# Kernel tuning notes

Hardware: AMD Instinct MI355X
Metric: run time of the kernel (lower is better)

## Reference

```python
import jax, jax.numpy as jnp
import numpy as np

NB_NODE = 100000
FT = 256
OUT_FT = 256
NB_REL = 4
BATCH = 8192
DEG = 16  # padded neighbors per (node, relation)


def setup_inputs() -> dict:
    key = jax.random.key(0)
    k1, k2, k3, k4 = jax.random.split(key, 4)
    features = jax.random.normal(k1, (NB_NODE, FT), dtype=jnp.float32)
    neighbor_idx = jax.random.randint(k2, (BATCH, NB_REL, DEG), 0, NB_NODE, dtype=jnp.int32)
    # per-relation GCN weight, scaled like xavier
    W = jax.random.normal(k3, (NB_REL, FT, OUT_FT), dtype=jnp.float32) * (1.0 / np.sqrt(FT))
    b = jnp.zeros((NB_REL, OUT_FT), dtype=jnp.float32)
    prelu_a = jnp.full((1,), 0.25, dtype=jnp.float32)  # nn.PReLU() default single param
    node_list = jax.random.randint(k4, (BATCH,), 0, NB_NODE, dtype=jnp.int32)
    return {"features": features, "neighbor_idx": neighbor_idx, "W": W, "b": b,
            "prelu_a": prelu_a, "node_list": node_list, "k": 0}


def _prelu(x, a):
    return jnp.where(x >= 0, x, a * x)


def reference(features, neighbor_idx, W, b, prelu_a, node_list, k):
    # Ragged per-relation neighbor gather + mean (vectorized form of the
    # python double loop): [B, R, D, F] -> mean over D -> [B, R, F]
    v_in = jnp.mean(features[neighbor_idx], axis=2)
    # Per-relation GCN linear + PReLU: [B, R, F] x [R, F, O] -> [B, R, O]
    h = jnp.einsum('brf,rfo->bro', v_in, W) + b[None, :, :]
    h = _prelu(h, prelu_a[0])
    # isAtt=False branch: mean over relations -> [B, O]
    return jnp.mean(h, axis=1)
```

## Files before the change

kernel.cpp:

```cpp
#include <hip/hip_runtime.h>

#define B_TOT 8192
#define FT    256
#define NREL  4
#define DEG   16
#define BM    16

typedef __attribute__((ext_vector_type(8))) short bf16x8;
typedef __attribute__((ext_vector_type(4))) float f32x4;

static __device__ __forceinline__ unsigned short f2bf(float x) {
    union { float f; unsigned int u; } c; c.f = x;
    unsigned int u = c.u;
    u += 0x7fffu + ((u >> 16) & 1u);
    return (unsigned short)(u >> 16);
}
static __device__ __forceinline__ float bf2f(unsigned short h) {
    union { unsigned int u; float f; } c; c.u = ((unsigned int)h) << 16;
    return c.f;
}

__global__ __launch_bounds__(256) void cvt_feat_k(const float* __restrict__ f,
                                                  unsigned short* __restrict__ fb,
                                                  int n4) {
    int i = blockIdx.x * 256 + threadIdx.x;
    if (i < n4) {
        float4 x = ((const float4*)f)[i];
        ushort4 o;
        o.x = f2bf(x.x); o.y = f2bf(x.y); o.z = f2bf(x.z); o.w = f2bf(x.w);
        ((ushort4*)fb)[i] = o;
    }
}

__global__ __launch_bounds__(256) void wtrans_k(const float* __restrict__ W,
                                                unsigned short* __restrict__ Wt) {
    __shared__ float t[64][65];
    int r = blockIdx.z, ft = blockIdx.y, ot = blockIdx.x;
    int c = threadIdx.x & 63, rw = threadIdx.x >> 6;
    const float* src = W + ((size_t)r * 256 + ft * 64) * 256 + ot * 64;
#pragma unroll
    for (int i = 0; i < 16; ++i) {
        int row = i * 4 + rw;
        t[row][c] = src[(size_t)row * 256 + c];
    }
    __syncthreads();
    unsigned short* dst = Wt + ((size_t)r * 256 + ot * 64) * 256 + ft * 64;
#pragma unroll
    for (int i = 0; i < 16; ++i) {
        int row = i * 4 + rw;
        dst[(size_t)row * 256 + c] = f2bf(t[c][row]);
    }
}

__global__ __launch_bounds__(512, 4) void fused_dma_k(const unsigned short* __restrict__ fb,
                                                      const int* __restrict__ nidx,
                                                      const unsigned short* __restrict__ Wt,
                                                      const float* __restrict__ bias,
                                                      const float* __restrict__ prelu,
                                                      float* __restrict__ out) {
    __shared__ int shIdx[BM * NREL * DEG];
    __shared__ unsigned short raw[8][2][1024];
    __shared__ unsigned short As[NREL][BM][FT + 8];
    const int tid  = threadIdx.x;
    const int lane = tid & 63, w = tid >> 6;
    const int l32  = lane & 31, half = lane >> 5;
    const int mrow = lane & 15, quad = lane >> 4;
    const int blk  = blockIdx.x;
    const float pa = prelu[0];

    ((int2*)shIdx)[tid] = ((const int2*)(nidx + (size_t)blk * (BM * NREL * DEG)))[tid];
    __syncthreads();

    const int mbase = w * 2;
    auto issue = [&](int c) {
        const int g = c >> 2, sub = c & 3;
        const int m = mbase + (g & 1), rel = g >> 1;
        const int* ib = shIdx + (m * NREL + rel) * DEG + sub * 4;
        unsigned short* slot = &raw[w][c & 1][0];
        const unsigned short* gA = fb + (size_t)ib[half]     * FT + l32 * 8;
        const unsigned short* gB = fb + (size_t)ib[2 + half] * FT + l32 * 8;
        __builtin_amdgcn_global_load_lds(
            (const __attribute__((address_space(1))) void*)gA,
            (__attribute__((address_space(3))) void*)&slot[lane * 8], 16, 0, 0);
        __builtin_amdgcn_global_load_lds(
            (const __attribute__((address_space(1))) void*)gB,
            (__attribute__((address_space(3))) void*)&slot[512 + lane * 8], 16, 0, 0);
    };

    float s0 = 0.f, s1 = 0.f, s2 = 0.f, s3 = 0.f;
    const float inv = 1.0f / 16.0f;
    issue(0);
#pragma unroll
    for (int c = 0; c < 32; ++c) {
        if (c + 1 < 32) issue(c + 1);
        if (c + 1 < 32) asm volatile("s_waitcnt vmcnt(2)" ::: "memory");
        else            asm volatile("s_waitcnt vmcnt(0)" ::: "memory");
        if ((c & 3) == 0) { s0 = s1 = s2 = s3 = 0.f; }
        const unsigned short* slot = &raw[w][c & 1][0];
#pragma unroll
        for (int j = 0; j < 4; ++j) {
            const ushort4 x = *(const ushort4*)(slot + j * 256 + lane * 4);
            s0 += bf2f(x.x); s1 += bf2f(x.y); s2 += bf2f(x.z); s3 += bf2f(x.w);
        }
        if ((c & 3) == 3) {
            const int g = c >> 2;
            const int m = mbase + (g & 1), rel = g >> 1;
            ushort4 o;
            o.x = f2bf(s0 * inv); o.y = f2bf(s1 * inv);
            o.z = f2bf(s2 * inv); o.w = f2bf(s3 * inv);
            *(ushort4*)(&As[rel][m][lane * 4]) = o;
        }
    }
    __syncthreads();

    const int ncol0 = w * 32 + mrow;
    f32x4 accO[2] = {};
#pragma unroll
    for (int r = 0; r < NREL; ++r) {
        const unsigned short* bp0 = Wt + ((size_t)(r * 256 + ncol0)) * FT;
        const unsigned short* bp1 = bp0 + 16 * FT;
        const float bv0 = bias[r * 256 + ncol0];
        const float bv1 = bias[r * 256 + ncol0 + 16];
        f32x4 acc[2] = {};
#pragma unroll
        for (int kk = 0; kk < 8; ++kk) {
            const int k0 = kk * 32 + quad * 8;
            const bf16x8 a  = *(const bf16x8*)(&As[r][mrow][k0]);
            const bf16x8 b0 = *(const bf16x8*)(bp0 + k0);
            const bf16x8 b1 = *(const bf16x8*)(bp1 + k0);
            acc[0] = __builtin_amdgcn_mfma_f32_16x16x32_bf16(a, b0, acc[0], 0, 0, 0);
            acc[1] = __builtin_amdgcn_mfma_f32_16x16x32_bf16(a, b1, acc[1], 0, 0, 0);
        }
#pragma unroll
        for (int i = 0; i < 4; ++i) {
            float h0 = acc[0][i] + bv0; h0 = (h0 >= 0.f) ? h0 : pa * h0;
            float h1 = acc[1][i] + bv1; h1 = (h1 >= 0.f) ? h1 : pa * h1;
            accO[0][i] += h0;
            accO[1][i] += h1;
        }
    }

    const size_t rbase = (size_t)(blk * BM + quad * 4) * 256 + ncol0;
#pragma unroll
    for (int i = 0; i < 4; ++i) {
        out[rbase + (size_t)i * 256]      = accO[0][i] * 0.25f;
        out[rbase + (size_t)i * 256 + 16] = accO[1][i] * 0.25f;
    }
}

__global__ __launch_bounds__(1024, 8) void fused_reg_k(const float* __restrict__ ff,
                                                       const int* __restrict__ nidx,
                                                       const unsigned short* __restrict__ Wt,
                                                       const float* __restrict__ bias,
                                                       const float* __restrict__ prelu,
                                                       float* __restrict__ out) {
    __shared__ int shIdx[BM * NREL * DEG];
    __shared__ unsigned short As[NREL][BM][FT + 8];
    const int tid  = threadIdx.x;
    const int lane = tid & 63, w = tid >> 6;
    const int blk  = blockIdx.x;
    const int mrow = lane & 15, quad = lane >> 4;
    const float pa = prelu[0];

    shIdx[tid] = nidx[(size_t)blk * (BM * NREL * DEG) + tid];
    __syncthreads();

    const float inv = 1.0f / 16.0f;
#pragma unroll
    for (int rr = 0; rr < NREL; ++rr) {
        const int* ip = shIdx + (w * NREL + rr) * DEG;
        float s0 = 0.f, s1 = 0.f, s2 = 0.f, s3 = 0.f;
#pragma unroll
        for (int h = 0; h < 2; ++h) {
            float4 x[8];
#pragma unroll
            for (int t = 0; t < 8; ++t)
                x[t] = ((const float4*)(ff + (size_t)ip[h * 8 + t] * FT))[lane];
#pragma unroll
            for (int t = 0; t < 8; ++t) {
                s0 += x[t].x; s1 += x[t].y; s2 += x[t].z; s3 += x[t].w;
            }
        }
        ushort4 o;
        o.x = f2bf(s0 * inv); o.y = f2bf(s1 * inv);
        o.z = f2bf(s2 * inv); o.w = f2bf(s3 * inv);
        *(ushort4*)(&As[rr][w][lane * 4]) = o;
    }
    __syncthreads();

    const int ncol = w * 16 + mrow;
    f32x4 accO = {};
#pragma unroll
    for (int r = 0; r < NREL; ++r) {
        const unsigned short* bp = Wt + ((size_t)(r * 256 + ncol)) * FT;
        const float bv = bias[r * 256 + ncol];
        f32x4 acc = {};
#pragma unroll
        for (int kk = 0; kk < 8; ++kk) {
            const int k0 = kk * 32 + quad * 8;
            const bf16x8 a = *(const bf16x8*)(&As[r][mrow][k0]);
            const bf16x8 b = *(const bf16x8*)(bp + k0);
            acc = __builtin_amdgcn_mfma_f32_16x16x32_bf16(a, b, acc, 0, 0, 0);
        }
#pragma unroll
        for (int i = 0; i < 4; ++i) {
            float h = acc[i] + bv;
            h = (h >= 0.f) ? h : pa * h;
            accO[i] += h;
        }
    }
    const size_t rbase = (size_t)(blk * BM + quad * 4) * 256 + ncol;
#pragma unroll
    for (int i = 0; i < 4; ++i)
        out[rbase + (size_t)i * 256] = accO[i] * 0.25f;
}

extern "C" void kernel_launch(void* const* d_in, const int* in_sizes, int n_in,
                              void* d_out, int out_size, void* d_ws, size_t ws_size,
                              hipStream_t stream) {
    const float* feat  = (const float*)d_in[0];
    const int*   nidx  = (const int*)  d_in[1];
    const float* W     = (const float*)d_in[2];
    const float* bias  = (const float*)d_in[3];
    const float* prelu = (const float*)d_in[4];
    float* out = (float*)d_out;

    const size_t feat_elems = (size_t)in_sizes[0];
    const size_t fb_bytes = feat_elems * 2;
    const size_t wt_bytes = (size_t)NREL * 256 * FT * 2;

    if (ws_size >= fb_bytes + wt_bytes) {
        unsigned short* fb = (unsigned short*)d_ws;
        unsigned short* Wt = fb + feat_elems;
        int n4 = (int)(feat_elems / 4);
        cvt_feat_k<<<(n4 + 255) / 256, 256, 0, stream>>>(feat, fb, n4);
        wtrans_k<<<dim3(4, 4, 4), 256, 0, stream>>>(W, Wt);
        fused_dma_k<<<B_TOT / BM, 512, 0, stream>>>(fb, nidx, Wt, bias, prelu, out);
    } else {
        unsigned short* Wt = (unsigned short*)d_ws;
        wtrans_k<<<dim3(4, 4, 4), 256, 0, stream>>>(W, Wt);
        fused_reg_k<<<B_TOT / BM, 1024, 0, stream>>>(feat, nidx, Wt, bias, prelu, out);
    }
}
```

Baseline: 230.2 us.

## Replace double-buffered LDS DMA gather with batched register gather of 16 neighbors

```diff
diff --git a/kernel.cpp b/kernel.cpp
--- a/kernel.cpp
+++ b/kernel.cpp
@@ -52,18 +52,16 @@
     }
 }
 
-__global__ __launch_bounds__(512, 4) void fused_dma_k(const unsigned short* __restrict__ fb,
-                                                      const int* __restrict__ nidx,
-                                                      const unsigned short* __restrict__ Wt,
-                                                      const float* __restrict__ bias,
-                                                      const float* __restrict__ prelu,
-                                                      float* __restrict__ out) {
+__global__ __launch_bounds__(512, 4) void fused_k(const unsigned short* __restrict__ fb,
+                                                  const int* __restrict__ nidx,
+                                                  const unsigned short* __restrict__ Wt,
+                                                  const float* __restrict__ bias,
+                                                  const float* __restrict__ prelu,
+                                                  float* __restrict__ out) {
     __shared__ int shIdx[BM * NREL * DEG];
-    __shared__ unsigned short raw[8][2][1024];
     __shared__ unsigned short As[NREL][BM][FT + 8];
     const int tid  = threadIdx.x;
     const int lane = tid & 63, w = tid >> 6;
-    const int l32  = lane & 31, half = lane >> 5;
     const int mrow = lane & 15, quad = lane >> 4;
     const int blk  = blockIdx.x;
     const float pa = prelu[0];
@@ -71,45 +69,33 @@
     ((int2*)shIdx)[tid] = ((const int2*)(nidx + (size_t)blk * (BM * NREL * DEG)))[tid];
     __syncthreads();
 
-    const int mbase = w * 2;
-    auto issue = [&](int c) {
-        const int g = c >> 2, sub = c & 3;
-        const int m = mbase + (g & 1), rel = g >> 1;
-        const int* ib = shIdx + (m * NREL + rel) * DEG + sub * 4;
-        unsigned short* slot = &raw[w][c & 1][0];
-        const unsigned short* gA = fb + (size_t)ib[half]     * FT + l32 * 8;
-        const unsigned short* gB = fb + (size_t)ib[2 + half] * FT + l32 * 8;
-        __builtin_amdgcn_global_load_lds(
-            (const __attribute__((address_space(1))) void*)gA,
-            (__attribute__((address_space(3))) void*)&slot[lane * 8], 16, 0, 0);
-        __builtin_amdgcn_global_load_lds(
-            (const __attribute__((address_space(1))) void*)gB,
-            (__attribute__((address_space(3))) void*)&slot[512 + lane * 8], 16, 0, 0);
-    };
-
-    float s0 = 0.f, s1 = 0.f, s2 = 0.f, s3 = 0.f;
     const float inv = 1.0f / 16.0f;
-    issue(0);
-#pragma unroll
-    for (int c = 0; c < 32; ++c) {
-        if (c + 1 < 32) issue(c + 1);
-        if (c + 1 < 32) asm volatile("s_waitcnt vmcnt(2)" ::: "memory");
-        else            asm volatile("s_waitcnt vmcnt(0)" ::: "memory");
-        if ((c & 3) == 0) { s0 = s1 = s2 = s3 = 0.f; }
-        const unsigned short* slot = &raw[w][c & 1][0];
-#pragma unroll
-        for (int j = 0; j < 4; ++j) {
-            const ushort4 x = *(const ushort4*)(slot + j * 256 + lane * 4);
-            s0 += bf2f(x.x); s1 += bf2f(x.y); s2 += bf2f(x.z); s3 += bf2f(x.w);
-        }
-        if ((c & 3) == 3) {
-            const int g = c >> 2;
-            const int m = mbase + (g & 1), rel = g >> 1;
-            ushort4 o;
-            o.x = f2bf(s0 * inv); o.y = f2bf(s1 * inv);
-            o.z = f2bf(s2 * inv); o.w = f2bf(s3 * inv);
-            *(ushort4*)(&As[rel][m][lane * 4]) = o;
-        }
+#pragma unroll
+    for (int t = 0; t < 8; ++t) {
+        const int g   = w * 8 + t;
+        const int m   = g >> 2, rel = g & 3;
+        const int* ip = shIdx + g * DEG;
+        const int4 i0 = *(const int4*)(ip);
+        const int4 i1 = *(const int4*)(ip + 4);
+        const int4 i2 = *(const int4*)(ip + 8);
+        const int4 i3 = *(const int4*)(ip + 12);
+        int idx[DEG] = { i0.x, i0.y, i0.z, i0.w, i1.x, i1.y, i1.z, i1.w,
+                         i2.x, i2.y, i2.z, i2.w, i3.x, i3.y, i3.z, i3.w };
+        ushort4 x[DEG];
+#pragma unroll
+        for (int j = 0; j < DEG; ++j)
+            x[j] = *(const ushort4*)(fb + (size_t)idx[j] * FT + lane * 4);
+        __builtin_amdgcn_sched_barrier(0);
+        float s0 = 0.f, s1 = 0.f, s2 = 0.f, s3 = 0.f;
+#pragma unroll
+        for (int j = 0; j < DEG; ++j) {
+            s0 += bf2f(x[j].x); s1 += bf2f(x[j].y);
+            s2 += bf2f(x[j].z); s3 += bf2f(x[j].w);
+        }
+        ushort4 o;
+        o.x = f2bf(s0 * inv); o.y = f2bf(s1 * inv);
+        o.z = f2bf(s2 * inv); o.w = f2bf(s3 * inv);
+        *(ushort4*)(&As[rel][m][lane * 4]) = o;
     }
     __syncthreads();
 
@@ -235,7 +221,7 @@
         int n4 = (int)(feat_elems / 4);
         cvt_feat_k<<<(n4 + 255) / 256, 256, 0, stream>>>(feat, fb, n4);
         wtrans_k<<<dim3(4, 4, 4), 256, 0, stream>>>(W, Wt);
-        fused_dma_k<<<B_TOT / BM, 512, 0, stream>>>(fb, nidx, Wt, bias, prelu, out);
+        fused_k<<<B_TOT / BM, 512, 0, stream>>>(fb, nidx, Wt, bias, prelu, out);
     } else {
         unsigned short* Wt = (unsigned short*)d_ws;
         wtrans_k<<<dim3(4, 4, 4), 256, 0, stream>>>(W, Wt);
```

After: 226.1 us. Within noise of the previous version (-1.8%).
